# Kernel optimization log

Hardware: AMD Instinct MI355X
Metric: run time of the kernel (lower is better)

The kernel has to match this reference:

```python
import jax, jax.numpy as jnp
import numpy as np

N_HEADS = 16
SEG_LEN = 512
MSG_LEN = 1536
T_TOTAL = SEG_LEN + MSG_LEN  # 2048


def _build_mask(T):
    # rows < SEG_LEN: attend to all cols < SEG_LEN (full, non-causal block)
    # rows >= SEG_LEN: standard causal (cols <= row)
    rows = jnp.arange(T)[:, None]
    cols = jnp.arange(T)[None, :]
    mask = jnp.where(rows < SEG_LEN, cols < SEG_LEN, cols <= rows)
    return mask  # [T, T] bool


def setup_inputs() -> dict:
    key = jax.random.key(0)
    k1, k2, k3 = jax.random.split(key, 3)
    B, T, E = 4, T_TOTAL, 1024
    x = jax.random.normal(k1, (B, T, E), dtype=jnp.float32)
    W_qkv = jax.random.normal(k2, (E, 3 * E), dtype=jnp.float32) * (1.0 / np.sqrt(E))
    b_qkv = jnp.zeros((3 * E,), dtype=jnp.float32)
    W_proj = jax.random.normal(k3, (E, E), dtype=jnp.float32) * (1.0 / np.sqrt(E))
    b_proj = jnp.zeros((E,), dtype=jnp.float32)
    return {"x": x, "W_qkv": W_qkv, "b_qkv": b_qkv, "W_proj": W_proj, "b_proj": b_proj}


def reference(x, W_qkv, b_qkv, W_proj, b_proj):
    B, T, E = x.shape
    H = N_HEADS
    D = E // H
    qkv = x @ W_qkv + b_qkv  # [B, T, 3E]
    q, k, v = jnp.split(qkv, 3, axis=-1)
    # [B, H, T, D]
    q = q.reshape(B, T, H, D).transpose(0, 2, 1, 3)
    k = k.reshape(B, T, H, D).transpose(0, 2, 1, 3)
    v = v.reshape(B, T, H, D).transpose(0, 2, 1, 3)
    att = jnp.einsum("bhqd,bhkd->bhqk", q, k) * (1.0 / np.sqrt(D))
    mask = _build_mask(T)  # [T, T]
    att = jnp.where(mask[None, None], att, jnp.float32(-jnp.inf))
    att = jax.nn.softmax(att, axis=-1)
    y = jnp.einsum("bhqk,bhkd->bhqd", att, v)
    y = y.transpose(0, 2, 1, 3).reshape(B, T, E)
    return y @ W_proj + b_proj
```

## Files before the change

kernel.cpp:

```cpp
#include <hip/hip_runtime.h>


typedef _Float16 f16;
typedef _Float16 f16x4 __attribute__((ext_vector_type(4)));
typedef _Float16 f16x8 __attribute__((ext_vector_type(8)));
typedef float f32x4 __attribute__((ext_vector_type(4)));

#define MFMA16x32(a, b, c) __builtin_amdgcn_mfma_f32_16x16x32_f16(a, b, c, 0, 0, 0)
#define MFMA16x16(a, b, c) __builtin_amdgcn_mfma_f32_16x16x16f16(a, b, c, 0, 0, 0)

__device__ __forceinline__ void gload_lds16(const void* g, void* l) {
  __builtin_amdgcn_global_load_lds(
      (__attribute__((address_space(1))) void*)g,
      (__attribute__((address_space(3))) void*)l, 16, 0, 0);
}


__global__ void k_cast_f16(const float* __restrict__ x, f16* __restrict__ xh) {
  int i = blockIdx.x * 256 + threadIdx.x;
  float4 v = ((const float4*)x)[i];
  f16x4 o = {(f16)v.x, (f16)v.y, (f16)v.z, (f16)v.w};
  ((f16x4*)xh)[i] = o;
}

__global__ void k_transpose(const float* __restrict__ W, f16* __restrict__ Wt,
                            int Kdim, int Ndim) {
  __shared__ float tile[32][33];
  int n = blockIdx.x * 32 + threadIdx.x;
  int k0 = blockIdx.y * 32;
  for (int j = threadIdx.y; j < 32; j += 8)
    tile[j][threadIdx.x] = W[(size_t)(k0 + j) * Ndim + n];
  __syncthreads();
  int k = k0 + threadIdx.x;
  for (int j = threadIdx.y; j < 32; j += 8)
    Wt[(size_t)(blockIdx.x * 32 + j) * Kdim + k] = (f16)tile[threadIdx.x][j];
}


__global__ __launch_bounds__(256) void k_gemm_qkv(
    const f16* __restrict__ A, const f16* __restrict__ Bt,
    const float* __restrict__ bias,
    f16* __restrict__ Qo, f16* __restrict__ Ko, f16* __restrict__ Vo) {
  constexpr int KD = 1024;
  __shared__ __align__(16) f16 As[128 * 32];
  __shared__ __align__(16) f16 Bs[128 * 32];
  __shared__ __align__(16) f16 Esh[4 * 64 * 72];
  const int tid = threadIdx.x;
  const int wave = tid >> 6, lane = tid & 63;
  const int g = lane >> 4, l16 = lane & 15;
  const int m0 = blockIdx.y * 128, n0 = blockIdx.x * 128;
  const int wm = (wave >> 1) * 64, wn = (wave & 1) * 64;
  const int srow = wave * 16 + (lane >> 2);
  const int skc = (lane & 3) * 8;

  f32x4 acc[4][4] = {};

  for (int k0 = 0; k0 < KD; k0 += 32) {
    __syncthreads();
    for (int it = 0; it < 2; ++it) {
      gload_lds16(A + (size_t)(m0 + it * 64 + srow) * KD + k0 + skc,
                  As + (it * 64 + wave * 16) * 32);
      gload_lds16(Bt + (size_t)(n0 + it * 64 + srow) * KD + k0 + skc,
                  Bs + (it * 64 + wave * 16) * 32);
    }
    __syncthreads();
    f16x8 af[4], bf[4];
    for (int mi = 0; mi < 4; ++mi)
      af[mi] = *(const f16x8*)(As + (wm + mi * 16 + l16) * 32 + g * 8);
    for (int ni = 0; ni < 4; ++ni)
      bf[ni] = *(const f16x8*)(Bs + (wn + ni * 16 + l16) * 32 + g * 8);
    for (int mi = 0; mi < 4; ++mi)
      for (int ni = 0; ni < 4; ++ni)
        acc[mi][ni] = MFMA16x32(af[mi], bf[ni], acc[mi][ni]);
  }

  const int nsub = n0 + wn;
  const int part = nsub >> 10;
  const int h    = (nsub >> 6) & 15;
  const int mg   = m0 + wm;
  const int b    = mg >> 11;
  const int tb   = mg & 2047;
  const size_t bh = (size_t)(b * 16 + h);
  f16* Es = Esh + wave * (64 * 72);

  float bv[4];
  for (int ni = 0; ni < 4; ++ni) bv[ni] = bias[nsub + ni * 16 + l16];

  for (int mi = 0; mi < 4; ++mi)
    for (int ni = 0; ni < 4; ++ni)
      for (int r = 0; r < 4; ++r) {
        f16 hv = (f16)(acc[mi][ni][r] + bv[ni]);
        int mrow = mi * 16 + g * 4 + r, ncol = ni * 16 + l16;
        if (part == 2) Es[ncol * 72 + mrow] = hv;
        else           Es[mrow * 72 + ncol] = hv;
      }

  const int rrow = lane >> 3, rcol = (lane & 7) * 8;
  for (int p = 0; p < 8; ++p) {
    int row = p * 8 + rrow;
    f16x8 vv = *(const f16x8*)(Es + row * 72 + rcol);
    if (part == 0)
      *(f16x8*)(Qo + (bh * 2048 + tb + row) * 64 + rcol) = vv;
    else if (part == 1)
      *(f16x8*)(Ko + (bh * 2048 + tb + row) * 64 + rcol) = vv;
    else
      *(f16x8*)(Vo + (bh * 64 + row) * 2048 + tb + rcol) = vv;
  }
}


__global__ __launch_bounds__(256, 3) void k_attn(
    const f16* __restrict__ Q, const f16* __restrict__ Kb,
    const f16* __restrict__ Vt, f16* __restrict__ Y) {
  __shared__ __align__(16) f16 Ks[64 * 64];
  __shared__ __align__(16) f16 Vs[64 * 64];

  const int tid = threadIdx.x;
  const int wave = tid >> 6, lane = tid & 63;
  const int g = lane >> 4, l16 = lane & 15;
  const int bh = blockIdx.y;
  const int q0 = (15 - blockIdx.x) * 128;

  f16x8 aq[2][2];
  for (int mi = 0; mi < 2; ++mi) {
    const f16* qrow =
        Q + ((size_t)bh * 2048 + q0 + wave * 32 + mi * 16 + l16) * 64 + g * 8;
    aq[mi][0] = *(const f16x8*)(qrow);
    aq[mi][1] = *(const f16x8*)(qrow + 32);
    for (int kb = 0; kb < 2; ++kb)
      aq[mi][kb] = aq[mi][kb] * (f16)0.18033688f;
  }

  f32x4 o[2][4] = {};
  float rsum[2] = {};
  const int niter = ((q0 < 512) ? 512 : (q0 + 128)) >> 6;
  const int srowrel = lane >> 3;
  const int sc = (lane & 7) ^ srowrel;

  const f32x4 sinit = {-8.65617025f, -8.65617025f, -8.65617025f, -8.65617025f};

  for (int i = 0; i < niter; ++i) {
    const int kt0 = i << 6;
    __syncthreads();
    for (int it = 0; it < 2; ++it) {
      int row = it * 32 + wave * 8 + srowrel;
      gload_lds16(Kb + ((size_t)bh * 2048 + kt0 + row) * 64 + sc * 8,
                  Ks + (it * 32 + wave * 8) * 64);
      gload_lds16(Vt + ((size_t)bh * 64 + row) * 2048 + kt0 + sc * 8,
                  Vs + (it * 32 + wave * 8) * 64);
    }
    __syncthreads();

    f32x4 t[2][4];
    for (int nb = 0; nb < 4; ++nb) {
      int R = nb * 16 + l16, sw = R & 7;
      f16x8 bk0 = *(const f16x8*)(Ks + R * 64 + ((0 + g) ^ sw) * 8);
      f16x8 bk1 = *(const f16x8*)(Ks + R * 64 + ((4 + g) ^ sw) * 8);
      for (int mi = 0; mi < 2; ++mi) {
        f32x4 acc = MFMA16x32(bk0, aq[mi][0], sinit);
        t[mi][nb] = MFMA16x32(bk1, aq[mi][1], acc);
      }
    }

    const bool masked = (q0 >= 512) && (kt0 >= q0);
    f16x4 ap[4][2];
    for (int mi = 0; mi < 2; ++mi) {
      const int mrow = q0 + wave * 32 + mi * 16 + l16;
      for (int nb = 0; nb < 4; ++nb)
        for (int r = 0; r < 4; ++r) {
          float p = __builtin_amdgcn_exp2f(t[mi][nb][r]);
          if (masked && (kt0 + nb * 16 + g * 4 + r > mrow)) p = 0.f;
          rsum[mi] += p;
          ap[nb][mi][r] = (f16)p;
        }
    }

    for (int db = 0; db < 4; ++db)
      for (int nb = 0; nb < 4; ++nb) {
        int R = db * 16 + l16, sw = R & 7;
        int c = nb * 2 + (g >> 1);
        f16x4 bv = *(const f16x4*)(Vs + R * 64 + (c ^ sw) * 8 + (g & 1) * 4);
        for (int mi = 0; mi < 2; ++mi)
          o[mi][db] = MFMA16x16(ap[nb][mi], bv, o[mi][db]);
      }
  }

  for (int mi = 0; mi < 2; ++mi) {
    rsum[mi] += __shfl_xor(rsum[mi], 16, 64);
    rsum[mi] += __shfl_xor(rsum[mi], 32, 64);
  }

  int b = bh >> 4, h = bh & 15;
  for (int mi = 0; mi < 2; ++mi)
    for (int r = 0; r < 4; ++r) {
      float rs = __shfl(rsum[mi], (lane & 48) + g * 4 + r, 64);
      float rinv = 1.0f / rs;
      size_t rowg = (size_t)b * 2048 + q0 + wave * 32 + mi * 16 + g * 4 + r;
      for (int db = 0; db < 4; ++db)
        Y[rowg * 1024 + h * 64 + db * 16 + l16] = (f16)(o[mi][db][r] * rinv);
    }
}


__global__ __launch_bounds__(256) void k_gemm_proj(
    const f16* __restrict__ A, const f16* __restrict__ Bt,
    const float* __restrict__ bias, float* __restrict__ out) {
  constexpr int KD = 1024;
  __shared__ __align__(16) f16 As[128 * 32];
  __shared__ __align__(16) f16 Bs[128 * 32];
  const int tid = threadIdx.x;
  const int wave = tid >> 6, lane = tid & 63;
  const int g = lane >> 4, l16 = lane & 15;
  const int m0 = blockIdx.y * 128, n0 = blockIdx.x * 128;
  const int wm = (wave >> 1) * 64, wn = (wave & 1) * 64;
  const int srow = wave * 16 + (lane >> 2);
  const int skc = (lane & 3) * 8;

  f32x4 acc[4][4] = {};

  for (int k0 = 0; k0 < KD; k0 += 32) {
    __syncthreads();
    for (int it = 0; it < 2; ++it) {
      gload_lds16(A + (size_t)(m0 + it * 64 + srow) * KD + k0 + skc,
                  As + (it * 64 + wave * 16) * 32);
      gload_lds16(Bt + (size_t)(n0 + it * 64 + srow) * KD + k0 + skc,
                  Bs + (it * 64 + wave * 16) * 32);
    }
    __syncthreads();
    f16x8 af[4], bf[4];
    for (int mi = 0; mi < 4; ++mi)
      af[mi] = *(const f16x8*)(As + (wm + mi * 16 + l16) * 32 + g * 8);
    for (int ni = 0; ni < 4; ++ni)
      bf[ni] = *(const f16x8*)(Bs + (wn + ni * 16 + l16) * 32 + g * 8);
    for (int mi = 0; mi < 4; ++mi)
      for (int ni = 0; ni < 4; ++ni)
        acc[mi][ni] = MFMA16x32(af[mi], bf[ni], acc[mi][ni]);
  }

  float bv[4];
  for (int ni = 0; ni < 4; ++ni) bv[ni] = bias[n0 + wn + ni * 16 + l16];

  for (int mi = 0; mi < 4; ++mi)
    for (int ni = 0; ni < 4; ++ni)
      for (int r = 0; r < 4; ++r) {
        int m = m0 + wm + mi * 16 + g * 4 + r;
        int n = n0 + wn + ni * 16 + l16;
        out[(size_t)m * 1024 + n] = acc[mi][ni][r] + bv[ni];
      }
}


extern "C" void kernel_launch(void* const* d_in, const int* in_sizes, int n_in,
                              void* d_out, int out_size, void* d_ws,
                              size_t ws_size, hipStream_t stream) {
  const float* x      = (const float*)d_in[0];
  const float* W_qkv  = (const float*)d_in[1];
  const float* b_qkv  = (const float*)d_in[2];
  const float* W_proj = (const float*)d_in[3];
  const float* b_proj = (const float*)d_in[4];
  float* out = (float*)d_out;

  char* ws = (char*)d_ws;
  f16* xh  = (f16*)ws; ws += (size_t)8192 * 1024 * 2;
  f16* Wqt = (f16*)ws; ws += (size_t)3072 * 1024 * 2;
  f16* Wpt = (f16*)ws; ws += (size_t)1024 * 1024 * 2;
  f16* Qb  = (f16*)ws; ws += (size_t)64 * 2048 * 64 * 2;
  f16* Kb  = (f16*)ws; ws += (size_t)64 * 2048 * 64 * 2;
  f16* Vt  = (f16*)ws; ws += (size_t)64 * 64 * 2048 * 2;
  f16* Y   = xh;

  k_cast_f16<<<8192, 256, 0, stream>>>(x, xh);
  k_transpose<<<dim3(96, 32), dim3(32, 8), 0, stream>>>(W_qkv, Wqt, 1024, 3072);
  k_transpose<<<dim3(32, 32), dim3(32, 8), 0, stream>>>(W_proj, Wpt, 1024, 1024);
  k_gemm_qkv<<<dim3(24, 64), 256, 0, stream>>>(xh, Wqt, b_qkv, Qb, Kb, Vt);
  k_attn<<<dim3(16, 64), 256, 0, stream>>>(Qb, Kb, Vt, Y);
  k_gemm_proj<<<dim3(8, 64), 256, 0, stream>>>(Y, Wpt, b_proj, out);
}
```

Before: 306.2 us.

## Split attention key range across blocks with atomic fp32 accumulation and combine pass

Each query tile's key range is split into chunks of up to eight 64-key tiles via constant lookup tables, giving 40 blocks per head instead of 16 and evening out the causal workload. Partial unnormalized outputs and row sums are atomically added into fp32 workspace buffers, and a new combine kernel normalizes them and writes f16 Y. The split works because softmax uses a fixed max offset, so partials can be summed directly. The cost is a memset, a 32MB fp32 atomic traffic stream, and an extra kernel launch, alongside a raised occupancy hint of 4.

```diff
diff --git a/kernel.cpp b/kernel.cpp
--- a/kernel.cpp
+++ b/kernel.cpp
@@ -109,9 +109,19 @@
 }
 
 
-__global__ __launch_bounds__(256, 3) void k_attn(
+__constant__ unsigned char cQT[40] = {0, 1, 2,  3,  4,  4,  5,  5,  6,  6,
+                                      7, 7, 8,  8,  8,  9,  9,  9,  10, 10,
+                                      10, 11, 11, 11, 12, 12, 12, 12, 13, 13,
+                                      13, 13, 14, 14, 14, 14, 15, 15, 15, 15};
+__constant__ unsigned char cC0[40] = {0, 0, 0, 0,  0, 8, 0, 8, 0, 8,
+                                      0, 8, 0, 8,  16, 0, 8, 16, 0, 8,
+                                      16, 0, 8, 16, 0, 8, 16, 24, 0, 8,
+                                      16, 24, 0, 8, 16, 24, 0, 8, 16, 24};
+
+__global__ __launch_bounds__(256, 4) void k_attn(
     const f16* __restrict__ Q, const f16* __restrict__ Kb,
-    const f16* __restrict__ Vt, f16* __restrict__ Y) {
+    const f16* __restrict__ Vt, float* __restrict__ Oacc,
+    float* __restrict__ Rsum) {
   __shared__ __align__(16) f16 Ks[64 * 64];
   __shared__ __align__(16) f16 Vs[64 * 64];
 
@@ -119,7 +129,11 @@
   const int wave = tid >> 6, lane = tid & 63;
   const int g = lane >> 4, l16 = lane & 15;
   const int bh = blockIdx.y;
-  const int q0 = (15 - blockIdx.x) * 128;
+  const int qt = cQT[blockIdx.x];
+  const int c0 = cC0[blockIdx.x];
+  const int q0 = qt * 128;
+  const int nt = (qt < 4) ? 8 : (qt + 1) * 2;
+  const int it_n = min(8, nt - c0);
 
   f16x8 aq[2][2];
   for (int mi = 0; mi < 2; ++mi) {
@@ -133,14 +147,13 @@
 
   f32x4 o[2][4] = {};
   float rsum[2] = {};
-  const int niter = ((q0 < 512) ? 512 : (q0 + 128)) >> 6;
   const int srowrel = lane >> 3;
   const int sc = (lane & 7) ^ srowrel;
 
   const f32x4 sinit = {-8.65617025f, -8.65617025f, -8.65617025f, -8.65617025f};
 
-  for (int i = 0; i < niter; ++i) {
-    const int kt0 = i << 6;
+  for (int i = 0; i < it_n; ++i) {
+    const int kt0 = (c0 + i) << 6;
     __syncthreads();
     for (int it = 0; it < 2; ++it) {
       int row = it * 32 + wave * 8 + srowrel;
@@ -190,15 +203,31 @@
     rsum[mi] += __shfl_xor(rsum[mi], 32, 64);
   }
 
+  const size_t rowbase = (size_t)bh * 2048 + q0 + wave * 32;
+  if (lane < 16)
+    for (int mi = 0; mi < 2; ++mi)
+      atomicAdd(&Rsum[rowbase + mi * 16 + l16], rsum[mi]);
+  for (int mi = 0; mi < 2; ++mi)
+    for (int db = 0; db < 4; ++db)
+      for (int r = 0; r < 4; ++r)
+        atomicAdd(&Oacc[(rowbase + mi * 16 + g * 4 + r) * 64 + db * 16 + l16],
+                  o[mi][db][r]);
+}
+
+
+__global__ void k_combine(const float* __restrict__ Oacc,
+                          const float* __restrict__ Rsum,
+                          f16* __restrict__ Y) {
+  int i = blockIdx.x * 256 + threadIdx.x;
+  int d4 = i & 15;
+  int t = (i >> 4) & 2047;
+  int bh = i >> 15;
+  float4 v = ((const float4*)Oacc)[i];
+  float rinv = 1.0f / Rsum[(bh << 11) + t];
   int b = bh >> 4, h = bh & 15;
-  for (int mi = 0; mi < 2; ++mi)
-    for (int r = 0; r < 4; ++r) {
-      float rs = __shfl(rsum[mi], (lane & 48) + g * 4 + r, 64);
-      float rinv = 1.0f / rs;
-      size_t rowg = (size_t)b * 2048 + q0 + wave * 32 + mi * 16 + g * 4 + r;
-      for (int db = 0; db < 4; ++db)
-        Y[rowg * 1024 + h * 64 + db * 16 + l16] = (f16)(o[mi][db][r] * rinv);
-    }
+  f16x4 ov = {(f16)(v.x * rinv), (f16)(v.y * rinv), (f16)(v.z * rinv),
+              (f16)(v.w * rinv)};
+  *(f16x4*)(Y + ((size_t)(b * 2048 + t) * 1024 + h * 64 + d4 * 4)) = ov;
 }
 
 
@@ -261,18 +290,24 @@
   float* out = (float*)d_out;
 
   char* ws = (char*)d_ws;
-  f16* xh  = (f16*)ws; ws += (size_t)8192 * 1024 * 2;
-  f16* Wqt = (f16*)ws; ws += (size_t)3072 * 1024 * 2;
-  f16* Wpt = (f16*)ws; ws += (size_t)1024 * 1024 * 2;
-  f16* Qb  = (f16*)ws; ws += (size_t)64 * 2048 * 64 * 2;
-  f16* Kb  = (f16*)ws; ws += (size_t)64 * 2048 * 64 * 2;
-  f16* Vt  = (f16*)ws; ws += (size_t)64 * 64 * 2048 * 2;
-  f16* Y   = xh;
+  f16* xh    = (f16*)ws;   ws += (size_t)8192 * 1024 * 2;
+  f16* Wqt   = (f16*)ws;   ws += (size_t)3072 * 1024 * 2;
+  f16* Wpt   = (f16*)ws;   ws += (size_t)1024 * 1024 * 2;
+  f16* Qb    = (f16*)ws;   ws += (size_t)64 * 2048 * 64 * 2;
+  f16* Kb    = (f16*)ws;   ws += (size_t)64 * 2048 * 64 * 2;
+  f16* Vt    = (f16*)ws;   ws += (size_t)64 * 64 * 2048 * 2;
+  float* Oacc = (float*)ws; ws += (size_t)64 * 2048 * 64 * 4;
+  float* Rsum = (float*)ws; ws += (size_t)64 * 2048 * 4;
+  f16* Y = xh;
+
+  hipMemsetAsync(Oacc, 0, (size_t)64 * 2048 * 64 * 4 + (size_t)64 * 2048 * 4,
+                 stream);
 
   k_cast_f16<<<8192, 256, 0, stream>>>(x, xh);
   k_transpose<<<dim3(96, 32), dim3(32, 8), 0, stream>>>(W_qkv, Wqt, 1024, 3072);
   k_transpose<<<dim3(32, 32), dim3(32, 8), 0, stream>>>(W_proj, Wpt, 1024, 1024);
   k_gemm_qkv<<<dim3(24, 64), 256, 0, stream>>>(xh, Wqt, b_qkv, Qb, Kb, Vt);
-  k_attn<<<dim3(16, 64), 256, 0, stream>>>(Qb, Kb, Vt, Y);
+  k_attn<<<dim3(40, 64), 256, 0, stream>>>(Qb, Kb, Vt, Oacc, Rsum);
+  k_combine<<<8192, 256, 0, stream>>>(Oacc, Rsum, Y);
   k_gemm_proj<<<dim3(8, 64), 256, 0, stream>>>(Y, Wpt, b_proj, out);
 }
```

Result: faster. 296.9 us (-3.0%).
